# Kernel tuning notes

Hardware: AMD Instinct MI355X
Metric: run time of the kernel (lower is better)

## Reference

```python
import jax, jax.numpy as jnp
import numpy as np

EXP_SCALE = 10.0   # self.exp_param_scale
BETA_UP = 5.0      # self.kernel_beta_upbound
N_HEAD = 12


def setup_inputs() -> dict:
    key = jax.random.key(0)
    ks = jax.random.split(key, 7)
    B, T, C, nh = 2, 2048, 768, N_HEAD
    s = 1.0 / np.sqrt(C)
    x = jax.random.normal(ks[0], (B, T, C), jnp.float32)
    W_la = jax.random.normal(ks[1], (C, C), jnp.float32) * s      # LeakyAverage linear
    la_coef = jax.random.uniform(ks[2], (nh,), jnp.float32)        # per-head leaky decay in (0,1)
    W_v = jax.random.normal(ks[3], (C, C), jnp.float32) * s        # v_featurizer linear
    v_coef = jax.random.uniform(ks[4], (nh,), jnp.float32)         # v_featurizer per-head coef
    kernel_beta = jnp.ones((nh,), jnp.float32) / EXP_SCALE
    value_beta = jnp.ones((nh,), jnp.float32) * (-0.5 / EXP_SCALE)
    W_proj = jax.random.normal(ks[5], (C, C), jnp.float32) * s     # c_proj
    return dict(x=x, W_la=W_la, la_coef=la_coef, W_v=W_v, v_coef=v_coef,
                kernel_beta=kernel_beta, value_beta=value_beta, W_proj=W_proj)


def _leaky_average(x, W_la, la_coef):
    # y_t = c * y_{t-1} + (1-c) * (x W^T)_t, per-head decay c. Returns (B, nh, T, hs).
    B, T, C = x.shape
    nh = la_coef.shape[0]
    hs = C // nh
    u = (x @ W_la.T).reshape(B, T, nh, hs)
    c = la_coef[None, :, None]  # (1, nh, 1) broadcast over (B, nh, hs)

    def step(carry, ut):
        y = c * carry + (1.0 - c) * ut
        return y, y

    _, ys = jax.lax.scan(step, jnp.zeros((B, nh, hs), x.dtype), jnp.swapaxes(u, 0, 1))
    return jnp.transpose(ys, (1, 2, 0, 3))  # (T,B,nh,hs) -> (B,nh,T,hs)


def reference(x, W_la, la_coef, W_v, v_coef, kernel_beta, value_beta, W_proj):
    B, T, C = x.shape
    nh = la_coef.shape[0]
    hs = C // nh
    v_shift = 1

    # K path: leaky-average features, L2-normalize, exp-kernel beta scale
    k0 = _leaky_average(x, W_la, la_coef)                               # (B,nh,T,hs)
    raw_k = k0 / (jnp.linalg.norm(k0, axis=-1, keepdims=True) + 1e-6)
    beta = jnp.exp(jnp.minimum(kernel_beta * EXP_SCALE, BETA_UP))
    k = raw_k * beta[None, :, None, None]

    # V path: lowrlinearconv featurizer (linear, shift-by-1 mix, normalize) + value scale
    xl = (x @ W_v.T).reshape(B, T, nh, hs).transpose(0, 2, 1, 3)        # (B,nh,T,hs)
    shifted = jnp.concatenate([xl[:, :, 1:], jnp.zeros_like(xl[:, :, :1])], axis=2)
    vc = v_coef[None, :, None, None]
    vf = shifted * (1.0 - vc) + xl * vc
    vf = vf / (jnp.linalg.norm(vf, axis=-1, keepdims=True) + 1e-6)
    vbeta = jnp.exp(jnp.minimum(value_beta * EXP_SCALE, BETA_UP))
    v = vf * vbeta[None, :, None, None]

    # shifted-causal attention: query at position t (t>=1) attends keys 0..t-1, scale=1.0
    q = k[:, :, v_shift:]                                               # (B,nh,T-1,hs)
    scores = jnp.einsum('bhqd,bhkd->bhqk', q, k)                        # (B,nh,T-1,T)
    mask = jnp.tril(jnp.ones((T - v_shift, T), bool))                   # j <= iq  <=>  key < query pos
    scores = jnp.where(mask, scores, -jnp.inf)
    attn = jax.nn.softmax(scores, axis=-1)
    o = jnp.einsum('bhqk,bhkd->bhqd', attn, v)
    y = jnp.concatenate([jnp.zeros((B, nh, v_shift, hs), x.dtype), o], axis=2)

    y = y.transpose(0, 2, 1, 3).reshape(B, T, C)
    return y @ W_proj.T  # c_proj (dropouts are identity in eval)
```

## Files before the change

kernel.cpp:

```cpp
#include <hip/hip_runtime.h>
#include <hip/hip_bf16.h>
#include <math.h>

#define B_   2
#define T_   2048
#define C_   768
#define NH   12
#define HS   64
#define NSEG 64
#define SEGLEN 32
#define CX   1536

typedef __attribute__((ext_vector_type(8))) short short8;
typedef __attribute__((ext_vector_type(4))) short short4v;
typedef __attribute__((ext_vector_type(4))) float f32x4;

static __device__ inline unsigned short f2b(float f) {
  __hip_bfloat16 h = __float2bfloat16(f);
  unsigned short u;
  __builtin_memcpy(&u, &h, 2);
  return u;
}
static __device__ inline float b2f(unsigned short u) {
  unsigned int x = ((unsigned int)u) << 16;
  float f;
  __builtin_memcpy(&f, &x, 4);
  return f;
}

#define GLOAD_LDS16(gp, lp)                                                        \
  __builtin_amdgcn_global_load_lds((const __attribute__((address_space(1))) void*)(gp), \
                                   (__attribute__((address_space(3))) void*)(lp), 16, 0, 0)

__global__ __launch_bounds__(256) void cast_all(const float* __restrict__ x,
                                                const float* __restrict__ wla,
                                                const float* __restrict__ wv,
                                                const float* __restrict__ wp,
                                                __hip_bfloat16* __restrict__ xb,
                                                __hip_bfloat16* __restrict__ wcat,
                                                __hip_bfloat16* __restrict__ wpb) {
  const int NX4 = (B_ * T_ * C_) / 4;
  const int NW4 = (C_ * C_) / 4;
  const int TOT = NX4 + 3 * NW4;
  int i = blockIdx.x * 256 + threadIdx.x;
  int st = gridDim.x * 256;
  for (; i < TOT; i += st) {
    const float* s;
    unsigned short* d;
    if (i < NX4) { s = x + (size_t)i * 4; d = (unsigned short*)xb + (size_t)i * 4; }
    else if (i < NX4 + NW4) { int j = i - NX4; s = wla + (size_t)j * 4; d = (unsigned short*)wcat + (size_t)j * 4; }
    else if (i < NX4 + 2 * NW4) { int j = i - NX4 - NW4; s = wv + (size_t)j * 4; d = (unsigned short*)wcat + (size_t)(C_ * C_) + (size_t)j * 4; }
    else { int j = i - NX4 - 2 * NW4; s = wp + (size_t)j * 4; d = (unsigned short*)wpb + (size_t)j * 4; }
    float4 v = *(const float4*)s;
    short4v o;
    o.x = (short)f2b(v.x); o.y = (short)f2b(v.y); o.z = (short)f2b(v.z); o.w = (short)f2b(v.w);
    *(short4v*)d = o;
  }
}

template <int BM, bool OB16>
__global__ __launch_bounds__(256) void gemm_bf16(const __hip_bfloat16* __restrict__ A,
                                                 const __hip_bfloat16* __restrict__ Bw,
                                                 void* __restrict__ Cv,
                                                 int M, int N, int K) {
  __shared__ __hip_bfloat16 As[BM * 64];
  __shared__ __hip_bfloat16 Bs[128 * 64];
  const int tid = threadIdx.x;
  const int w = tid >> 6, lane = tid & 63;
  const int bm = blockIdx.x * BM, bn = blockIdx.y * 128;
  const int q16 = lane & 15, lg = lane >> 4;

  constexpr int NACC = (BM == 128) ? 4 : 2;
  f32x4 acc[4][NACC];
#pragma unroll
  for (int i = 0; i < 4; ++i)
#pragma unroll
    for (int j = 0; j < NACC; ++j) acc[i][j] = (f32x4){0.f, 0.f, 0.f, 0.f};

  const int srow = (lane >> 3);
  const int soff0 = (lane & 7) * 16;
  const int sw = (lane & 7) << 4;
  constexpr int ACH = BM / 8;
  constexpr int CPW = (ACH + 16) / 4;

  for (int k0 = 0; k0 < K; k0 += 64) {
    __syncthreads();
#pragma unroll
    for (int c = 0; c < CPW; ++c) {
      int gc = w * CPW + c;
      int isB = gc >= ACH;
      int ci = isB ? gc - ACH : gc;
      int row = ci * 8 + srow;
      int soff = soff0 ^ ((row & 7) << 4);
      const __hip_bfloat16* gp =
          (isB ? Bw + (size_t)(bn + row) * K : A + (size_t)(bm + row) * K) + k0 + (soff >> 1);
      __hip_bfloat16* lp = (isB ? Bs : As) + ci * 512;
      GLOAD_LDS16(gp, lp);
    }
    __syncthreads();
#pragma unroll
    for (int ks = 0; ks < 2; ++ks) {
      short8 af[4], bf[NACC];
      const int colb = ks * 64 + lg * 16;
#pragma unroll
      for (int i = 0; i < 4; ++i) {
        int ra = (BM == 128) ? ((w >> 1) * 64 + i * 16 + q16) : (i * 16 + q16);
        af[i] = *(const short8*)((const char*)As + ra * 128 + (colb ^ sw));
      }
#pragma unroll
      for (int j = 0; j < NACC; ++j) {
        int rb = (BM == 128) ? ((w & 1) * 64 + j * 16 + q16) : (w * 32 + j * 16 + q16);
        bf[j] = *(const short8*)((const char*)Bs + rb * 128 + (colb ^ sw));
      }
#pragma unroll
      for (int i = 0; i < 4; ++i)
#pragma unroll
        for (int j = 0; j < NACC; ++j)
          acc[i][j] = __builtin_amdgcn_mfma_f32_16x16x32_bf16(af[i], bf[j], acc[i][j], 0, 0, 0);
    }
  }
#pragma unroll
  for (int i = 0; i < 4; ++i) {
#pragma unroll
    for (int r = 0; r < 4; ++r) {
      int m = (BM == 128) ? (bm + (w >> 1) * 64 + i * 16 + lg * 4 + r)
                          : (bm + i * 16 + lg * 4 + r);
      int nb = (BM == 128) ? (bn + (w & 1) * 64 + q16) : (bn + w * 32 + q16);
      if (OB16) {
        unsigned short* cp = (unsigned short*)Cv + (size_t)m * N + nb;
#pragma unroll
        for (int j = 0; j < NACC; ++j) cp[j * 16] = f2b(acc[i][j][r]);
      } else {
        float* cp = (float*)Cv + (size_t)m * N + nb;
#pragma unroll
        for (int j = 0; j < NACC; ++j) cp[j * 16] = acc[i][j][r];
      }
    }
  }
}

__global__ __launch_bounds__(256) void scan_seg(const unsigned short* __restrict__ uxv,
                                                const float* __restrict__ la_coef,
                                                float* __restrict__ segend) {
  int cid = blockIdx.x * 4 + (threadIdx.x >> 6);
  int d   = threadIdx.x & 63;
  int seg = cid & (NSEG - 1);
  int bh  = cid >> 6;
  int h   = bh % NH;
  int b   = bh / NH;
  float c  = la_coef[h];
  float oc = 1.f - c;
  int t0 = seg * SEGLEN;
  const unsigned short* up = uxv + ((size_t)b * T_ + t0) * CX + h * HS + d;
  float uv[SEGLEN];
#pragma unroll
  for (int i = 0; i < SEGLEN; ++i) uv[i] = b2f(up[(size_t)i * CX]);
  float y = 0.f;
#pragma unroll
  for (int i = 0; i < SEGLEN; ++i) y = fmaf(c, y, oc * uv[i]);
  segend[(size_t)cid * HS + d] = y;
}

__global__ __launch_bounds__(256) void scanc_vbuild(const float* __restrict__ la_coef,
                                                    const float* __restrict__ kernel_beta,
                                                    const float* __restrict__ segend,
                                                    const unsigned short* __restrict__ uxv,
                                                    const float* __restrict__ v_coef,
                                                    const float* __restrict__ value_beta,
                                                    __hip_bfloat16* __restrict__ kb16,
                                                    __hip_bfloat16* __restrict__ vt) {
  __shared__ __hip_bfloat16 sm[64][73];
  const int NBC = B_ * NH * NSEG / 4;
  if ((int)blockIdx.x < NBC) {
    int cid = blockIdx.x * 4 + (threadIdx.x >> 6);
    int d   = threadIdx.x & 63;
    int seg = cid & (NSEG - 1);
    int bh  = cid >> 6;
    int h   = bh % NH;
    int b   = bh / NH;
    float c  = la_coef[h];
    float oc = 1.f - c;
    float bk = __expf(fminf(kernel_beta[h] * 10.f, 5.f));
    float cl = c;
#pragma unroll
    for (int i = 0; i < 5; ++i) cl *= cl;
    const float* se = segend + (size_t)bh * NSEG * HS + d;
    float y = 0.f;
    for (int s = 0; s < seg; ++s) y = fmaf(y, cl, se[(size_t)s * HS]);
    int t0 = seg * SEGLEN;
    const unsigned short* up = uxv + ((size_t)b * T_ + t0) * CX + h * HS + d;
    __hip_bfloat16* op = kb16 + ((size_t)bh * T_ + t0) * HS + d;
    float uv[SEGLEN];
#pragma unroll
    for (int i = 0; i < SEGLEN; ++i) uv[i] = b2f(up[(size_t)i * CX]);
    for (int i = 0; i < SEGLEN; ++i) {
      y = fmaf(c, y, oc * uv[i]);
      float ss = y * y;
#pragma unroll
      for (int off = 1; off < 64; off <<= 1) ss += __shfl_xor(ss, off, 64);
      float scale = bk / (sqrtf(ss) + 1e-6f);
      op[(size_t)i * HS] = __float2bfloat16(y * scale);
    }
  } else {
    int idx = blockIdx.x - NBC;
    int t0 = (idx & 31) * 64;
    int bh = idx >> 5;
    int h = bh % NH, b = bh / NH;
    int w = threadIdx.x >> 6, lane = threadIdx.x & 63;
    float vc = v_coef[h];
    float vb = __expf(fminf(value_beta[h] * 10.f, 5.f));
    for (int i = 0; i < 16; ++i) {
      int tl = w * 16 + i;
      int t = t0 + tl;
      const unsigned short* xp = uxv + ((size_t)b * T_ + t) * CX + 768 + h * HS + lane;
      float x0 = b2f(*xp);
      float x1 = (t + 1 < T_) ? b2f(xp[CX]) : 0.f;
      float vf = (1.f - vc) * x1 + vc * x0;
      float ss = vf * vf;
#pragma unroll
      for (int off = 1; off < 64; off <<= 1) ss += __shfl_xor(ss, off, 64);
      sm[tl][lane] = __float2bfloat16(vf * vb / (sqrtf(ss) + 1e-6f));
    }
    __syncthreads();
    int d = threadIdx.x >> 3;
    int c = threadIdx.x & 7;
    for (int i = 0; i < 2; ++i) {
      int dd = d + i * 32;
      short8 v;
#pragma unroll
      for (int k = 0; k < 8; ++k)
        v[k] = (short)((const unsigned short*)&sm[c * 8 + k][dd])[0];
      *(short8*)((unsigned short*)vt + ((size_t)bh * HS + dd) * T_ + t0 + c * 8) = v;
    }
  }
}

__global__ __launch_bounds__(256, 2) void attn8(const __hip_bfloat16* __restrict__ Kg,
                                                const __hip_bfloat16* __restrict__ Vtg,
                                                const float* __restrict__ kernel_beta,
                                                __hip_bfloat16* __restrict__ Y) {
  __shared__ __align__(16) char lds[38912];
  const int bh = blockIdx.x;
  const int b = bh / NH, h = bh % NH;
  const int w = threadIdx.x >> 6, lane = threadIdx.x & 63;
  const int q16 = lane & 15, lg = lane >> 4;
  const int it = 31 - blockIdx.y;
  const int qb0 = 1 + it * 64;
  const int NT32 = 2 * it + 2;
  float bk = __expf(fminf(kernel_beta[h] * 10.f, 5.f));
  const float L2E = 1.4426950408889634f;
  const float m0l = bk * bk * L2E;
  const unsigned short* Kh = (const unsigned short*)Kg + (size_t)bh * T_ * HS;
  const unsigned short* Vh = (const unsigned short*)Vtg + (size_t)bh * HS * T_;
  unsigned short* Yh = (unsigned short*)Y + (size_t)b * T_ * C_ + h * HS;

  if (it == 0 && w == 0) Yh[lane] = 0;

  short8 qf[4][2];
#pragma unroll
  for (int qs = 0; qs < 4; ++qs) {
    int tqc = qb0 + qs * 16 + q16;
    if (tqc > T_ - 1) tqc = T_ - 1;
#pragma unroll
    for (int ks = 0; ks < 2; ++ks)
      qf[qs][ks] = *(const short8*)(Kh + (size_t)tqc * HS + ks * 32 + lg * 8);
  }

  f32x4 zero = {0.f, 0.f, 0.f, 0.f};
  f32x4 accO[4][4];
#pragma unroll
  for (int qs = 0; qs < 4; ++qs)
#pragma unroll
    for (int mt = 0; mt < 4; ++mt) accO[qs][mt] = zero;
  float lsum[4] = {0.f, 0.f, 0.f, 0.f};
  char* pwbase = lds + (size_t)w * 4 * 1152;

#define LOADT(KF, VF, j0)                                                             \
  {                                                                                   \
    _Pragma("unroll")                                                                 \
    for (int nt = 0; nt < 2; ++nt)                                                    \
      _Pragma("unroll")                                                               \
      for (int ks = 0; ks < 2; ++ks)                                                  \
        KF[nt][ks] = *(const short8*)(Kh + (size_t)((j0) + nt * 16 + q16) * HS +      \
                                      ks * 32 + lg * 8);                              \
    _Pragma("unroll")                                                                 \
    for (int mt = 0; mt < 4; ++mt)                                                    \
      VF[mt] = *(const short8*)(Vh + (size_t)(mt * 16 + q16) * T_ + (j0) + lg * 8);   \
  }

#define COMPUTE(KF, VF, ktv)                                                          \
  {                                                                                   \
    const int j0c = (ktv)*32;                                                         \
    _Pragma("unroll")                                                                 \
    for (int qs = 0; qs < 4; ++qs) {                                                  \
      const int tqq = qb0 + qs * 16 + q16;                                            \
      char* pb = pwbase + qs * 1152 + q16 * 72;                                       \
      f32x4 s0 = __builtin_amdgcn_mfma_f32_16x16x32_bf16(KF[0][0], qf[qs][0], zero, 0, 0, 0); \
      s0 = __builtin_amdgcn_mfma_f32_16x16x32_bf16(KF[0][1], qf[qs][1], s0, 0, 0, 0); \
      f32x4 s1 = __builtin_amdgcn_mfma_f32_16x16x32_bf16(KF[1][0], qf[qs][0], zero, 0, 0, 0); \
      s1 = __builtin_amdgcn_mfma_f32_16x16x32_bf16(KF[1][1], qf[qs][1], s1, 0, 0, 0); \
      float p0[4], p1[4];                                                             \
      _Pragma("unroll")                                                               \
      for (int r = 0; r < 4; ++r) {                                                   \
        int j0r = j0c + lg * 4 + r;                                                   \
        p0[r] = (j0r < tqq) ? exp2f(fmaf(s0[r], L2E, -m0l)) : 0.f;                    \
        int j1r = j0c + 16 + lg * 4 + r;                                              \
        p1[r] = (j1r < tqq) ? exp2f(fmaf(s1[r], L2E, -m0l)) : 0.f;                    \
        lsum[qs] += p0[r] + p1[r];                                                    \
      }                                                                               \
      unsigned int w00, w01, w10, w11;                                                \
      asm("v_cvt_pk_bf16_f32 %0, %1, %2" : "=v"(w00) : "v"(p0[0]), "v"(p0[1]));       \
      asm("v_cvt_pk_bf16_f32 %0, %1, %2" : "=v"(w01) : "v"(p0[2]), "v"(p0[3]));       \
      asm("v_cvt_pk_bf16_f32 %0, %1, %2" : "=v"(w10) : "v"(p1[0]), "v"(p1[1]));       \
      asm("v_cvt_pk_bf16_f32 %0, %1, %2" : "=v"(w11) : "v"(p1[2]), "v"(p1[3]));       \
      uint2 pkA; pkA.x = w00; pkA.y = w01;                                            \
      uint2 pkB; pkB.x = w10; pkB.y = w11;                                            \
      *(uint2*)(pb + lg * 8) = pkA;                                                   \
      *(uint2*)(pb + 32 + lg * 8) = pkB;                                              \
      short8 pf = *(const short8*)(pb + lg * 16);                                     \
      _Pragma("unroll")                                                               \
      for (int mt = 0; mt < 4; ++mt)                                                  \
        accO[qs][mt] = __builtin_amdgcn_mfma_f32_16x16x32_bf16(VF[mt], pf, accO[qs][mt], 0, 0, 0); \
    }                                                                                 \
  }

  short8 kfA[2][2], vfA[4], kfB[2][2], vfB[4];
  int kt = w;
  if (kt < NT32) LOADT(kfA, vfA, kt * 32);
  while (kt < NT32) {
    if (kt + 4 < NT32) LOADT(kfB, vfB, (kt + 4) * 32);
    COMPUTE(kfA, vfA, kt);
    kt += 4;
    if (kt >= NT32) break;
    if (kt + 4 < NT32) LOADT(kfA, vfA, (kt + 4) * 32);
    COMPUTE(kfB, vfB, kt);
    kt += 4;
  }

  __syncthreads();
  float* LR = (float*)(lds + 34816);
  if (w >= 2) {
    float* PB = (float*)(lds + (size_t)(w - 2) * 17408);
#pragma unroll
    for (int qs = 0; qs < 4; ++qs)
#pragma unroll
      for (int mt = 0; mt < 4; ++mt)
        *(f32x4*)(PB + (qs * 16 + q16) * 68 + mt * 16 + lg * 4) = accO[qs][mt];
  }
#pragma unroll
  for (int qs = 0; qs < 4; ++qs)
    LR[((size_t)w * 64 + qs * 16 + q16) * 4 + lg] = lsum[qs];
  __syncthreads();
  if (w < 2) {
    float* PB = (float*)(lds + (size_t)w * 17408);
#pragma unroll
    for (int qs = 0; qs < 4; ++qs)
#pragma unroll
      for (int mt = 0; mt < 4; ++mt) {
        f32x4 o = *(f32x4*)(PB + (qs * 16 + q16) * 68 + mt * 16 + lg * 4);
        accO[qs][mt][0] += o[0]; accO[qs][mt][1] += o[1];
        accO[qs][mt][2] += o[2]; accO[qs][mt][3] += o[3];
      }
    if (w == 1) {
#pragma unroll
      for (int qs = 0; qs < 4; ++qs)
#pragma unroll
        for (int mt = 0; mt < 4; ++mt)
          *(f32x4*)(PB + (qs * 16 + q16) * 68 + mt * 16 + lg * 4) = accO[qs][mt];
    }
  }
  __syncthreads();
  if (w == 0) {
    float* PB1 = (float*)(lds + 17408);
#pragma unroll
    for (int qs = 0; qs < 4; ++qs) {
#pragma unroll
      for (int mt = 0; mt < 4; ++mt) {
        f32x4 o = *(f32x4*)(PB1 + (qs * 16 + q16) * 68 + mt * 16 + lg * 4);
        accO[qs][mt][0] += o[0]; accO[qs][mt][1] += o[1];
        accO[qs][mt][2] += o[2]; accO[qs][mt][3] += o[3];
      }
      float tot = 0.f;
#pragma unroll
      for (int p = 0; p < 4; ++p) {
        f32x4 lv = *(f32x4*)(LR + ((size_t)p * 64 + qs * 16 + q16) * 4);
        tot += lv[0] + lv[1] + lv[2] + lv[3];
      }
      float inv = 1.f / tot;
      int tq = qb0 + qs * 16 + q16;
      if (tq < T_) {
        unsigned short* yp = Yh + (size_t)tq * C_;
#pragma unroll
        for (int mt = 0; mt < 4; ++mt) {
          float o0 = accO[qs][mt][0] * inv, o1 = accO[qs][mt][1] * inv;
          float o2 = accO[qs][mt][2] * inv, o3 = accO[qs][mt][3] * inv;
          unsigned int u0, u1;
          asm("v_cvt_pk_bf16_f32 %0, %1, %2" : "=v"(u0) : "v"(o0), "v"(o1));
          asm("v_cvt_pk_bf16_f32 %0, %1, %2" : "=v"(u1) : "v"(o2), "v"(o3));
          uint2 pk; pk.x = u0; pk.y = u1;
          *(uint2*)(yp + mt * 16 + lg * 4) = pk;
        }
      }
    }
  }
#undef LOADT
#undef COMPUTE
}

extern "C" void kernel_launch(void* const* d_in, const int* in_sizes, int n_in,
                              void* d_out, int out_size, void* d_ws, size_t ws_size,
                              hipStream_t stream) {
  const float* x          = (const float*)d_in[0];
  const float* W_la       = (const float*)d_in[1];
  const float* la_coef    = (const float*)d_in[2];
  const float* W_v        = (const float*)d_in[3];
  const float* v_coef     = (const float*)d_in[4];
  const float* kernel_bet = (const float*)d_in[5];
  const float* value_bet  = (const float*)d_in[6];
  const float* W_proj     = (const float*)d_in[7];
  float* out = (float*)d_out;

  char* ws = (char*)d_ws;
  const size_t NTOK = (size_t)B_ * T_ * C_;
  const size_t NSEGTOT = (size_t)B_ * NH * NSEG * HS;
  unsigned short* uxv = (unsigned short*)ws;
  float* segend  = (float*)(ws + (size_t)B_ * T_ * CX * 2);
  __hip_bfloat16* kb16 = (__hip_bfloat16*)(segend + NSEGTOT);
  __hip_bfloat16* vt16 = kb16 + NTOK;
  __hip_bfloat16* xb   = vt16 + NTOK;
  __hip_bfloat16* Wcat = xb + NTOK;
  __hip_bfloat16* Wpb  = Wcat + (size_t)CX * C_;
  __hip_bfloat16* yb   = xb;

  const int M = B_ * T_;

  cast_all<<<2048, 256, 0, stream>>>(x, W_la, W_v, W_proj, xb, Wcat, Wpb);

  gemm_bf16<64, true><<<dim3(M / 64, CX / 128), 256, 0, stream>>>(xb, Wcat, uxv, M, CX, C_);

  scan_seg<<<dim3(B_ * NH * NSEG / 4), 256, 0, stream>>>(uxv, la_coef, segend);
  scanc_vbuild<<<dim3(B_ * NH * NSEG / 4 + 32 * B_ * NH), 256, 0, stream>>>(
      la_coef, kernel_bet, segend, uxv, v_coef, value_bet, kb16, vt16);

  attn8<<<dim3(B_ * NH, 32), 256, 0, stream>>>(kb16, vt16, kernel_bet, yb);

  gemm_bf16<64, false><<<dim3(M / 64, C_ / 128), 256, 0, stream>>>(yb, Wpb, out, M, C_, C_);
}
```

Measured before the change: 110.3 us.

## Precompute scan carries, skip masking on full tiles, shrink attention LDS reduction

Adds a small kernel that computes each segment's carry-in state once, so each scan chunk no longer re-walks all prior segment ends serially. In the attention kernel, key tiles lying entirely below the causal diagonal skip the per-element mask comparisons. The cross-wave output reduction becomes a sequential accumulate through one shared buffer, which cuts LDS use so three blocks can fit per CU. The cost is an extra kernel launch and more barriers in the reduction.

```diff
diff --git a/kernel.cpp b/kernel.cpp
--- a/kernel.cpp
+++ b/kernel.cpp
@@ -161,9 +161,29 @@
   segend[(size_t)cid * HS + d] = y;
 }
 
+__global__ __launch_bounds__(256) void scan_b(const float* __restrict__ la_coef,
+                                              const float* __restrict__ segend,
+                                              float* __restrict__ carryin) {
+  int s = blockIdx.x * 256 + threadIdx.x;
+  if (s >= B_ * NH * HS) return;
+  int d  = s & 63;
+  int bh = s >> 6;
+  int h  = bh % NH;
+  float c = la_coef[h];
+  float cl = c;
+#pragma unroll
+  for (int i = 0; i < 5; ++i) cl *= cl;
+  float h0 = 0.f;
+  for (int seg = 0; seg < NSEG; ++seg) {
+    int cid = bh * NSEG + seg;
+    carryin[(size_t)cid * HS + d] = h0;
+    h0 = fmaf(cl, h0, segend[(size_t)cid * HS + d]);
+  }
+}
+
 __global__ __launch_bounds__(256) void scanc_vbuild(const float* __restrict__ la_coef,
                                                     const float* __restrict__ kernel_beta,
-                                                    const float* __restrict__ segend,
+                                                    const float* __restrict__ carryin,
                                                     const unsigned short* __restrict__ uxv,
                                                     const float* __restrict__ v_coef,
                                                     const float* __restrict__ value_beta,
@@ -181,18 +201,13 @@
     float c  = la_coef[h];
     float oc = 1.f - c;
     float bk = __expf(fminf(kernel_beta[h] * 10.f, 5.f));
-    float cl = c;
-#pragma unroll
-    for (int i = 0; i < 5; ++i) cl *= cl;
-    const float* se = segend + (size_t)bh * NSEG * HS + d;
-    float y = 0.f;
-    for (int s = 0; s < seg; ++s) y = fmaf(y, cl, se[(size_t)s * HS]);
     int t0 = seg * SEGLEN;
     const unsigned short* up = uxv + ((size_t)b * T_ + t0) * CX + h * HS + d;
     __hip_bfloat16* op = kb16 + ((size_t)bh * T_ + t0) * HS + d;
     float uv[SEGLEN];
 #pragma unroll
     for (int i = 0; i < SEGLEN; ++i) uv[i] = b2f(up[(size_t)i * CX]);
+    float y = carryin[(size_t)cid * HS + d];
     for (int i = 0; i < SEGLEN; ++i) {
       y = fmaf(c, y, oc * uv[i]);
       float ss = y * y;
@@ -235,11 +250,11 @@
   }
 }
 
-__global__ __launch_bounds__(256, 2) void attn8(const __hip_bfloat16* __restrict__ Kg,
+__global__ __launch_bounds__(256, 3) void attn9(const __hip_bfloat16* __restrict__ Kg,
                                                 const __hip_bfloat16* __restrict__ Vtg,
                                                 const float* __restrict__ kernel_beta,
                                                 __hip_bfloat16* __restrict__ Y) {
-  __shared__ __align__(16) char lds[38912];
+  __shared__ __align__(16) char lds[18432];
   const int bh = blockIdx.x;
   const int b = bh / NH, h = bh % NH;
   const int w = threadIdx.x >> 6, lane = threadIdx.x & 63;
@@ -294,19 +309,29 @@
     _Pragma("unroll")                                                                 \
     for (int qs = 0; qs < 4; ++qs) {                                                  \
       const int tqq = qb0 + qs * 16 + q16;                                            \
+      const bool unmasked = (j0c + 32 <= qb0 + qs * 16);            \
       char* pb = pwbase + qs * 1152 + q16 * 72;                                       \
       f32x4 s0 = __builtin_amdgcn_mfma_f32_16x16x32_bf16(KF[0][0], qf[qs][0], zero, 0, 0, 0); \
       s0 = __builtin_amdgcn_mfma_f32_16x16x32_bf16(KF[0][1], qf[qs][1], s0, 0, 0, 0); \
       f32x4 s1 = __builtin_amdgcn_mfma_f32_16x16x32_bf16(KF[1][0], qf[qs][0], zero, 0, 0, 0); \
       s1 = __builtin_amdgcn_mfma_f32_16x16x32_bf16(KF[1][1], qf[qs][1], s1, 0, 0, 0); \
       float p0[4], p1[4];                                                             \
-      _Pragma("unroll")                                                               \
-      for (int r = 0; r < 4; ++r) {                                                   \
-        int j0r = j0c + lg * 4 + r;                                                   \
-        p0[r] = (j0r < tqq) ? exp2f(fmaf(s0[r], L2E, -m0l)) : 0.f;                    \
-        int j1r = j0c + 16 + lg * 4 + r;                                              \
-        p1[r] = (j1r < tqq) ? exp2f(fmaf(s1[r], L2E, -m0l)) : 0.f;                    \
-        lsum[qs] += p0[r] + p1[r];                                                    \
+      if (unmasked) {                                                                 \
+        _Pragma("unroll")                                                             \
+        for (int r = 0; r < 4; ++r) {                                                 \
+          p0[r] = exp2f(fmaf(s0[r], L2E, -m0l));                                      \
+          p1[r] = exp2f(fmaf(s1[r], L2E, -m0l));                                      \
+          lsum[qs] += p0[r] + p1[r];                                                  \
+        }                                                                             \
+      } else {                                                                        \
+        _Pragma("unroll")                                                             \
+        for (int r = 0; r < 4; ++r) {                                                 \
+          int j0r = j0c + lg * 4 + r;                                                 \
+          p0[r] = (j0r < tqq) ? exp2f(fmaf(s0[r], L2E, -m0l)) : 0.f;                  \
+          int j1r = j0c + 16 + lg * 4 + r;                                            \
+          p1[r] = (j1r < tqq) ? exp2f(fmaf(s1[r], L2E, -m0l)) : 0.f;                  \
+          lsum[qs] += p0[r] + p1[r];                                                  \
+        }                                                                             \
       }                                                                               \
       unsigned int w00, w01, w10, w11;                                                \
       asm("v_cvt_pk_bf16_f32 %0, %1, %2" : "=v"(w00) : "v"(p0[0]), "v"(p0[1]));       \
@@ -338,55 +363,61 @@
   }
 
   __syncthreads();
-  float* LR = (float*)(lds + 34816);
-  if (w >= 2) {
-    float* PB = (float*)(lds + (size_t)(w - 2) * 17408);
-#pragma unroll
-    for (int qs = 0; qs < 4; ++qs)
+  float* PB = (float*)lds;
+  if (w == 3) {
+#pragma unroll
+    for (int qs = 0; qs < 4; ++qs) {
+      float* rb = PB + (qs * 16 + q16) * 72;
 #pragma unroll
       for (int mt = 0; mt < 4; ++mt)
-        *(f32x4*)(PB + (qs * 16 + q16) * 68 + mt * 16 + lg * 4) = accO[qs][mt];
-  }
-#pragma unroll
-  for (int qs = 0; qs < 4; ++qs)
-    LR[((size_t)w * 64 + qs * 16 + q16) * 4 + lg] = lsum[qs];
+        *(f32x4*)(rb + mt * 16 + lg * 4) = accO[qs][mt];
+      rb[64 + lg] = lsum[qs];
+    }
+  }
   __syncthreads();
-  if (w < 2) {
-    float* PB = (float*)(lds + (size_t)w * 17408);
-#pragma unroll
-    for (int qs = 0; qs < 4; ++qs)
+  if (w == 2) {
+#pragma unroll
+    for (int qs = 0; qs < 4; ++qs) {
+      float* rb = PB + (qs * 16 + q16) * 72;
 #pragma unroll
       for (int mt = 0; mt < 4; ++mt) {
-        f32x4 o = *(f32x4*)(PB + (qs * 16 + q16) * 68 + mt * 16 + lg * 4);
+        f32x4 o = *(f32x4*)(rb + mt * 16 + lg * 4);
+        o[0] += accO[qs][mt][0]; o[1] += accO[qs][mt][1];
+        o[2] += accO[qs][mt][2]; o[3] += accO[qs][mt][3];
+        *(f32x4*)(rb + mt * 16 + lg * 4) = o;
+      }
+      rb[64 + lg] += lsum[qs];
+    }
+  }
+  __syncthreads();
+  if (w == 1) {
+#pragma unroll
+    for (int qs = 0; qs < 4; ++qs) {
+      float* rb = PB + (qs * 16 + q16) * 72;
+#pragma unroll
+      for (int mt = 0; mt < 4; ++mt) {
+        f32x4 o = *(f32x4*)(rb + mt * 16 + lg * 4);
+        o[0] += accO[qs][mt][0]; o[1] += accO[qs][mt][1];
+        o[2] += accO[qs][mt][2]; o[3] += accO[qs][mt][3];
+        *(f32x4*)(rb + mt * 16 + lg * 4) = o;
+      }
+      rb[64 + lg] += lsum[qs];
+    }
+  }
+  __syncthreads();
+  if (w == 0) {
+#pragma unroll
+    for (int qs = 0; qs < 4; ++qs) {
+      float* rb = PB + (qs * 16 + q16) * 72;
+#pragma unroll
+      for (int mt = 0; mt < 4; ++mt) {
+        f32x4 o = *(f32x4*)(rb + mt * 16 + lg * 4);
         accO[qs][mt][0] += o[0]; accO[qs][mt][1] += o[1];
         accO[qs][mt][2] += o[2]; accO[qs][mt][3] += o[3];
       }
-    if (w == 1) {
-#pragma unroll
-      for (int qs = 0; qs < 4; ++qs)
-#pragma unroll
-        for (int mt = 0; mt < 4; ++mt)
-          *(f32x4*)(PB + (qs * 16 + q16) * 68 + mt * 16 + lg * 4) = accO[qs][mt];
-    }
-  }
-  __syncthreads();
-  if (w == 0) {
-    float* PB1 = (float*)(lds + 17408);
-#pragma unroll
-    for (int qs = 0; qs < 4; ++qs) {
-#pragma unroll
-      for (int mt = 0; mt < 4; ++mt) {
-        f32x4 o = *(f32x4*)(PB1 + (qs * 16 + q16) * 68 + mt * 16 + lg * 4);
-        accO[qs][mt][0] += o[0]; accO[qs][mt][1] += o[1];
-        accO[qs][mt][2] += o[2]; accO[qs][mt][3] += o[3];
-      }
-      float tot = 0.f;
-#pragma unroll
-      for (int p = 0; p < 4; ++p) {
-        f32x4 lv = *(f32x4*)(LR + ((size_t)p * 64 + qs * 16 + q16) * 4);
-        tot += lv[0] + lv[1] + lv[2] + lv[3];
-      }
-      float inv = 1.f / tot;
+      rb[64 + lg] += lsum[qs];
+      f32x4 lv = *(f32x4*)(rb + 64);
+      float inv = 1.f / (lv[0] + lv[1] + lv[2] + lv[3]);
       int tq = qb0 + qs * 16 + q16;
       if (tq < T_) {
         unsigned short* yp = Yh + (size_t)tq * C_;
@@ -425,7 +456,8 @@
   const size_t NSEGTOT = (size_t)B_ * NH * NSEG * HS;
   unsigned short* uxv = (unsigned short*)ws;
   float* segend  = (float*)(ws + (size_t)B_ * T_ * CX * 2);
-  __hip_bfloat16* kb16 = (__hip_bfloat16*)(segend + NSEGTOT);
+  float* carryin = segend + NSEGTOT;
+  __hip_bfloat16* kb16 = (__hip_bfloat16*)(carryin + NSEGTOT);
   __hip_bfloat16* vt16 = kb16 + NTOK;
   __hip_bfloat16* xb   = vt16 + NTOK;
   __hip_bfloat16* Wcat = xb + NTOK;
@@ -439,10 +471,11 @@
   gemm_bf16<64, true><<<dim3(M / 64, CX / 128), 256, 0, stream>>>(xb, Wcat, uxv, M, CX, C_);
 
   scan_seg<<<dim3(B_ * NH * NSEG / 4), 256, 0, stream>>>(uxv, la_coef, segend);
+  scan_b<<<dim3((B_ * NH * HS + 255) / 256), 256, 0, stream>>>(la_coef, segend, carryin);
   scanc_vbuild<<<dim3(B_ * NH * NSEG / 4 + 32 * B_ * NH), 256, 0, stream>>>(
-      la_coef, kernel_bet, segend, uxv, v_coef, value_bet, kb16, vt16);
-
-  attn8<<<dim3(B_ * NH, 32), 256, 0, stream>>>(kb16, vt16, kernel_bet, yb);
+      la_coef, kernel_bet, carryin, uxv, v_coef, value_bet, kb16, vt16);
+
+  attn9<<<dim3(B_ * NH, 32), 256, 0, stream>>>(kb16, vt16, kernel_bet, yb);
 
   gemm_bf16<64, false><<<dim3(M / 64, C_ / 128), 256, 0, stream>>>(yb, Wpb, out, M, C_, C_);
 }
```

Result: slower. 227.3 us (+106.1%).

## Switch attention to 32x32 MFMA with permlane P-reshuffle; precompute segment carries

Applied to the files above, without the earlier changes.

The attention kernel is rewritten to use 32x32x16 bf16 MFMAs over 32-query tiles. The softmax probabilities are rearranged into the B-operand layout with permlane32_swap in registers instead of a round trip through LDS, and s_setprio is placed around the MFMA groups. Separately, a new small scan kernel computes per-segment carry-in values once, so each scanc block no longer loops serially over all earlier segment ends. This adds one more kernel launch, and the larger accumulators raise register pressure.

```diff
diff --git a/kernel.cpp b/kernel.cpp
--- a/kernel.cpp
+++ b/kernel.cpp
@@ -14,6 +14,9 @@
 typedef __attribute__((ext_vector_type(8))) short short8;
 typedef __attribute__((ext_vector_type(4))) short short4v;
 typedef __attribute__((ext_vector_type(4))) float f32x4;
+typedef __attribute__((ext_vector_type(16))) float f32x16;
+typedef __attribute__((ext_vector_type(2))) unsigned int uint2v;
+typedef __attribute__((ext_vector_type(4))) unsigned int uint4v;
 
 static __device__ inline unsigned short f2b(float f) {
   __hip_bfloat16 h = __float2bfloat16(f);
@@ -26,6 +29,11 @@
   float f;
   __builtin_memcpy(&f, &x, 4);
   return f;
+}
+static __device__ inline unsigned cvtpk(float a, float b) {
+  unsigned r;
+  asm("v_cvt_pk_bf16_f32 %0, %1, %2" : "=v"(r) : "v"(a), "v"(b));
+  return r;
 }
 
 #define GLOAD_LDS16(gp, lp)                                                        \
@@ -161,9 +169,29 @@
   segend[(size_t)cid * HS + d] = y;
 }
 
+__global__ __launch_bounds__(256) void scan_b(const float* __restrict__ la_coef,
+                                              const float* __restrict__ segend,
+                                              float* __restrict__ carryin) {
+  int s = blockIdx.x * 256 + threadIdx.x;
+  if (s >= B_ * NH * HS) return;
+  int d  = s & 63;
+  int bh = s >> 6;
+  int h  = bh % NH;
+  float c = la_coef[h];
+  float cl = c;
+#pragma unroll
+  for (int i = 0; i < 5; ++i) cl *= cl;
+  float h0 = 0.f;
+  for (int seg = 0; seg < NSEG; ++seg) {
+    int cid = bh * NSEG + seg;
+    carryin[(size_t)cid * HS + d] = h0;
+    h0 = fmaf(cl, h0, segend[(size_t)cid * HS + d]);
+  }
+}
+
 __global__ __launch_bounds__(256) void scanc_vbuild(const float* __restrict__ la_coef,
                                                     const float* __restrict__ kernel_beta,
-                                                    const float* __restrict__ segend,
+                                                    const float* __restrict__ carryin,
                                                     const unsigned short* __restrict__ uxv,
                                                     const float* __restrict__ v_coef,
                                                     const float* __restrict__ value_beta,
@@ -181,18 +209,13 @@
     float c  = la_coef[h];
     float oc = 1.f - c;
     float bk = __expf(fminf(kernel_beta[h] * 10.f, 5.f));
-    float cl = c;
-#pragma unroll
-    for (int i = 0; i < 5; ++i) cl *= cl;
-    const float* se = segend + (size_t)bh * NSEG * HS + d;
-    float y = 0.f;
-    for (int s = 0; s < seg; ++s) y = fmaf(y, cl, se[(size_t)s * HS]);
     int t0 = seg * SEGLEN;
     const unsigned short* up = uxv + ((size_t)b * T_ + t0) * CX + h * HS + d;
     __hip_bfloat16* op = kb16 + ((size_t)bh * T_ + t0) * HS + d;
     float uv[SEGLEN];
 #pragma unroll
     for (int i = 0; i < SEGLEN; ++i) uv[i] = b2f(up[(size_t)i * CX]);
+    float y = carryin[(size_t)cid * HS + d];
     for (int i = 0; i < SEGLEN; ++i) {
       y = fmaf(c, y, oc * uv[i]);
       float ss = y * y;
@@ -235,15 +258,15 @@
   }
 }
 
-__global__ __launch_bounds__(256, 2) void attn8(const __hip_bfloat16* __restrict__ Kg,
-                                                const __hip_bfloat16* __restrict__ Vtg,
-                                                const float* __restrict__ kernel_beta,
-                                                __hip_bfloat16* __restrict__ Y) {
-  __shared__ __align__(16) char lds[38912];
+__global__ __launch_bounds__(256, 2) void attn10(const __hip_bfloat16* __restrict__ Kg,
+                                                 const __hip_bfloat16* __restrict__ Vtg,
+                                                 const float* __restrict__ kernel_beta,
+                                                 __hip_bfloat16* __restrict__ Y) {
+  __shared__ __align__(16) char lds[33792];
   const int bh = blockIdx.x;
   const int b = bh / NH, h = bh % NH;
   const int w = threadIdx.x >> 6, lane = threadIdx.x & 63;
-  const int q16 = lane & 15, lg = lane >> 4;
+  const int l31 = lane & 31, lg2 = lane >> 5;
   const int it = 31 - blockIdx.y;
   const int qb0 = 1 + it * 64;
   const int NT32 = 2 * it + 2;
@@ -256,75 +279,83 @@
 
   if (it == 0 && w == 0) Yh[lane] = 0;
 
-  short8 qf[4][2];
-#pragma unroll
-  for (int qs = 0; qs < 4; ++qs) {
-    int tqc = qb0 + qs * 16 + q16;
+  short8 qf[2][4];
+#pragma unroll
+  for (int qs = 0; qs < 2; ++qs) {
+    int tqc = qb0 + qs * 32 + l31;
     if (tqc > T_ - 1) tqc = T_ - 1;
 #pragma unroll
-    for (int ks = 0; ks < 2; ++ks)
-      qf[qs][ks] = *(const short8*)(Kh + (size_t)tqc * HS + ks * 32 + lg * 8);
-  }
-
-  f32x4 zero = {0.f, 0.f, 0.f, 0.f};
-  f32x4 accO[4][4];
-#pragma unroll
-  for (int qs = 0; qs < 4; ++qs)
-#pragma unroll
-    for (int mt = 0; mt < 4; ++mt) accO[qs][mt] = zero;
-  float lsum[4] = {0.f, 0.f, 0.f, 0.f};
-  char* pwbase = lds + (size_t)w * 4 * 1152;
+    for (int s = 0; s < 4; ++s)
+      qf[qs][s] = *(const short8*)(Kh + (size_t)tqc * HS + s * 16 + lg2 * 8);
+  }
+
+  f32x16 zero16 = {0.f};
+  f32x16 accO[2][2];
+#pragma unroll
+  for (int qs = 0; qs < 2; ++qs)
+#pragma unroll
+    for (int ds = 0; ds < 2; ++ds) accO[qs][ds] = zero16;
+  float lsum[2] = {0.f, 0.f};
 
 #define LOADT(KF, VF, j0)                                                             \
   {                                                                                   \
     _Pragma("unroll")                                                                 \
-    for (int nt = 0; nt < 2; ++nt)                                                    \
+    for (int s = 0; s < 4; ++s)                                                       \
+      KF[s] = *(const short8*)(Kh + (size_t)((j0) + l31) * HS + s * 16 + lg2 * 8);    \
+    _Pragma("unroll")                                                                 \
+    for (int ds = 0; ds < 2; ++ds)                                                    \
       _Pragma("unroll")                                                               \
-      for (int ks = 0; ks < 2; ++ks)                                                  \
-        KF[nt][ks] = *(const short8*)(Kh + (size_t)((j0) + nt * 16 + q16) * HS +      \
-                                      ks * 32 + lg * 8);                              \
-    _Pragma("unroll")                                                                 \
-    for (int mt = 0; mt < 4; ++mt)                                                    \
-      VF[mt] = *(const short8*)(Vh + (size_t)(mt * 16 + q16) * T_ + (j0) + lg * 8);   \
+      for (int s2 = 0; s2 < 2; ++s2)                                                  \
+        VF[ds][s2] = *(const short8*)(Vh + (size_t)(ds * 32 + l31) * T_ + (j0) +      \
+                                      s2 * 16 + lg2 * 8);                             \
   }
 
 #define COMPUTE(KF, VF, ktv)                                                          \
   {                                                                                   \
     const int j0c = (ktv)*32;                                                         \
+    const int jb = j0c + 4 * lg2;                                                     \
     _Pragma("unroll")                                                                 \
-    for (int qs = 0; qs < 4; ++qs) {                                                  \
-      const int tqq = qb0 + qs * 16 + q16;                                            \
-      char* pb = pwbase + qs * 1152 + q16 * 72;                                       \
-      f32x4 s0 = __builtin_amdgcn_mfma_f32_16x16x32_bf16(KF[0][0], qf[qs][0], zero, 0, 0, 0); \
-      s0 = __builtin_amdgcn_mfma_f32_16x16x32_bf16(KF[0][1], qf[qs][1], s0, 0, 0, 0); \
-      f32x4 s1 = __builtin_amdgcn_mfma_f32_16x16x32_bf16(KF[1][0], qf[qs][0], zero, 0, 0, 0); \
-      s1 = __builtin_amdgcn_mfma_f32_16x16x32_bf16(KF[1][1], qf[qs][1], s1, 0, 0, 0); \
-      float p0[4], p1[4];                                                             \
+    for (int qs = 0; qs < 2; ++qs) {                                                  \
+      const int tqq = qb0 + qs * 32 + l31;                                            \
+      f32x16 S = zero16;                                                              \
+      __builtin_amdgcn_s_setprio(1);                                                  \
       _Pragma("unroll")                                                               \
-      for (int r = 0; r < 4; ++r) {                                                   \
-        int j0r = j0c + lg * 4 + r;                                                   \
-        p0[r] = (j0r < tqq) ? exp2f(fmaf(s0[r], L2E, -m0l)) : 0.f;                    \
-        int j1r = j0c + 16 + lg * 4 + r;                                              \
-        p1[r] = (j1r < tqq) ? exp2f(fmaf(s1[r], L2E, -m0l)) : 0.f;                    \
-        lsum[qs] += p0[r] + p1[r];                                                    \
+      for (int s = 0; s < 4; ++s)                                                     \
+        S = __builtin_amdgcn_mfma_f32_32x32x16_bf16(KF[s], qf[qs][s], S, 0, 0, 0);    \
+      __builtin_amdgcn_s_setprio(0);                                                  \
+      float p[16];                                                                    \
+      _Pragma("unroll")                                                               \
+      for (int r = 0; r < 16; ++r) {                                                  \
+        int jg = jb + (r & 3) + 8 * (r >> 2);                                         \
+        p[r] = (jg < tqq) ? exp2f(fmaf(S[r], L2E, -m0l)) : 0.f;                       \
+        lsum[qs] += p[r];                                                             \
       }                                                                               \
-      unsigned int w00, w01, w10, w11;                                                \
-      asm("v_cvt_pk_bf16_f32 %0, %1, %2" : "=v"(w00) : "v"(p0[0]), "v"(p0[1]));       \
-      asm("v_cvt_pk_bf16_f32 %0, %1, %2" : "=v"(w01) : "v"(p0[2]), "v"(p0[3]));       \
-      asm("v_cvt_pk_bf16_f32 %0, %1, %2" : "=v"(w10) : "v"(p1[0]), "v"(p1[1]));       \
-      asm("v_cvt_pk_bf16_f32 %0, %1, %2" : "=v"(w11) : "v"(p1[2]), "v"(p1[3]));       \
-      uint2 pkA; pkA.x = w00; pkA.y = w01;                                            \
-      uint2 pkB; pkB.x = w10; pkB.y = w11;                                            \
-      *(uint2*)(pb + lg * 8) = pkA;                                                   \
-      *(uint2*)(pb + 32 + lg * 8) = pkB;                                              \
-      short8 pf = *(const short8*)(pb + lg * 16);                                     \
+      uint2v g00 = __builtin_amdgcn_permlane32_swap(cvtpk(p[0], p[1]),                \
+                                                    cvtpk(p[4], p[5]), false, false); \
+      uint2v g01 = __builtin_amdgcn_permlane32_swap(cvtpk(p[2], p[3]),                \
+                                                    cvtpk(p[6], p[7]), false, false); \
+      uint2v g10 = __builtin_amdgcn_permlane32_swap(cvtpk(p[8], p[9]),                \
+                                                    cvtpk(p[12], p[13]), false, false);\
+      uint2v g11 = __builtin_amdgcn_permlane32_swap(cvtpk(p[10], p[11]),              \
+                                                    cvtpk(p[14], p[15]), false, false);\
+      uint4v pb0v, pb1v;                                                              \
+      pb0v.x = g00.x; pb0v.y = g01.x; pb0v.z = g00.y; pb0v.w = g01.y;                 \
+      pb1v.x = g10.x; pb1v.y = g11.x; pb1v.z = g10.y; pb1v.w = g11.y;                 \
+      short8 PB0 = __builtin_bit_cast(short8, pb0v);                                  \
+      short8 PB1 = __builtin_bit_cast(short8, pb1v);                                  \
+      __builtin_amdgcn_s_setprio(1);                                                  \
       _Pragma("unroll")                                                               \
-      for (int mt = 0; mt < 4; ++mt)                                                  \
-        accO[qs][mt] = __builtin_amdgcn_mfma_f32_16x16x32_bf16(VF[mt], pf, accO[qs][mt], 0, 0, 0); \
+      for (int ds = 0; ds < 2; ++ds) {                                                \
+        accO[qs][ds] = __builtin_amdgcn_mfma_f32_32x32x16_bf16(VF[ds][0], PB0,        \
+                                                               accO[qs][ds], 0, 0, 0);\
+        accO[qs][ds] = __builtin_amdgcn_mfma_f32_32x32x16_bf16(VF[ds][1], PB1,        \
+                                                               accO[qs][ds], 0, 0, 0);\
+      }                                                                               \
+      __builtin_amdgcn_s_setprio(0);                                                  \
     }                                                                                 \
   }
 
-  short8 kfA[2][2], vfA[4], kfB[2][2], vfB[4];
+  short8 kfA[4], vfA[2][2], kfB[4], vfB[2][2];
   int kt = w;
   if (kt < NT32) LOADT(kfA, vfA, kt * 32);
   while (kt < NT32) {
@@ -337,69 +368,65 @@
     kt += 4;
   }
 
+#pragma unroll
+  for (int qs = 0; qs < 2; ++qs) lsum[qs] += __shfl_xor(lsum[qs], 32, 64);
+
+  float* LR = (float*)(lds + 32768);
   __syncthreads();
-  float* LR = (float*)(lds + 34816);
   if (w >= 2) {
-    float* PB = (float*)(lds + (size_t)(w - 2) * 17408);
-#pragma unroll
-    for (int qs = 0; qs < 4; ++qs)
-#pragma unroll
-      for (int mt = 0; mt < 4; ++mt)
-        *(f32x4*)(PB + (qs * 16 + q16) * 68 + mt * 16 + lg * 4) = accO[qs][mt];
-  }
-#pragma unroll
-  for (int qs = 0; qs < 4; ++qs)
-    LR[((size_t)w * 64 + qs * 16 + q16) * 4 + lg] = lsum[qs];
+    float* PB = (float*)(lds + (size_t)(w - 2) * 16384);
+#pragma unroll
+    for (int qs = 0; qs < 2; ++qs)
+#pragma unroll
+      for (int ds = 0; ds < 2; ++ds)
+        *(f32x16*)(PB + ((qs * 2 + ds) * 64 + lane) * 16) = accO[qs][ds];
+  }
+#pragma unroll
+  for (int qs = 0; qs < 2; ++qs) LR[(w * 2 + qs) * 32 + l31] = lsum[qs];
   __syncthreads();
   if (w < 2) {
-    float* PB = (float*)(lds + (size_t)w * 17408);
-#pragma unroll
-    for (int qs = 0; qs < 4; ++qs)
-#pragma unroll
-      for (int mt = 0; mt < 4; ++mt) {
-        f32x4 o = *(f32x4*)(PB + (qs * 16 + q16) * 68 + mt * 16 + lg * 4);
-        accO[qs][mt][0] += o[0]; accO[qs][mt][1] += o[1];
-        accO[qs][mt][2] += o[2]; accO[qs][mt][3] += o[3];
+    float* PB = (float*)(lds + (size_t)w * 16384);
+#pragma unroll
+    for (int qs = 0; qs < 2; ++qs)
+#pragma unroll
+      for (int ds = 0; ds < 2; ++ds) {
+        f32x16 o = *(f32x16*)(PB + ((qs * 2 + ds) * 64 + lane) * 16);
+#pragma unroll
+        for (int r = 0; r < 16; ++r) accO[qs][ds][r] += o[r];
       }
     if (w == 1) {
 #pragma unroll
-      for (int qs = 0; qs < 4; ++qs)
-#pragma unroll
-        for (int mt = 0; mt < 4; ++mt)
-          *(f32x4*)(PB + (qs * 16 + q16) * 68 + mt * 16 + lg * 4) = accO[qs][mt];
+      for (int qs = 0; qs < 2; ++qs)
+#pragma unroll
+        for (int ds = 0; ds < 2; ++ds)
+          *(f32x16*)(PB + ((qs * 2 + ds) * 64 + lane) * 16) = accO[qs][ds];
     }
   }
   __syncthreads();
   if (w == 0) {
-    float* PB1 = (float*)(lds + 17408);
-#pragma unroll
-    for (int qs = 0; qs < 4; ++qs) {
-#pragma unroll
-      for (int mt = 0; mt < 4; ++mt) {
-        f32x4 o = *(f32x4*)(PB1 + (qs * 16 + q16) * 68 + mt * 16 + lg * 4);
-        accO[qs][mt][0] += o[0]; accO[qs][mt][1] += o[1];
-        accO[qs][mt][2] += o[2]; accO[qs][mt][3] += o[3];
-      }
-      float tot = 0.f;
-#pragma unroll
-      for (int p = 0; p < 4; ++p) {
-        f32x4 lv = *(f32x4*)(LR + ((size_t)p * 64 + qs * 16 + q16) * 4);
-        tot += lv[0] + lv[1] + lv[2] + lv[3];
-      }
+    float* PB1 = (float*)(lds + 16384);
+#pragma unroll
+    for (int qs = 0; qs < 2; ++qs) {
+#pragma unroll
+      for (int ds = 0; ds < 2; ++ds) {
+        f32x16 o = *(f32x16*)(PB1 + ((qs * 2 + ds) * 64 + lane) * 16);
+#pragma unroll
+        for (int r = 0; r < 16; ++r) accO[qs][ds][r] += o[r];
+      }
+      float tot = LR[(0 * 2 + qs) * 32 + l31] + LR[(1 * 2 + qs) * 32 + l31] +
+                  LR[(2 * 2 + qs) * 32 + l31] + LR[(3 * 2 + qs) * 32 + l31];
       float inv = 1.f / tot;
-      int tq = qb0 + qs * 16 + q16;
+      int tq = qb0 + qs * 32 + l31;
       if (tq < T_) {
         unsigned short* yp = Yh + (size_t)tq * C_;
 #pragma unroll
-        for (int mt = 0; mt < 4; ++mt) {
-          float o0 = accO[qs][mt][0] * inv, o1 = accO[qs][mt][1] * inv;
-          float o2 = accO[qs][mt][2] * inv, o3 = accO[qs][mt][3] * inv;
-          unsigned int u0, u1;
-          asm("v_cvt_pk_bf16_f32 %0, %1, %2" : "=v"(u0) : "v"(o0), "v"(o1));
-          asm("v_cvt_pk_bf16_f32 %0, %1, %2" : "=v"(u1) : "v"(o2), "v"(o3));
-          uint2 pk; pk.x = u0; pk.y = u1;
-          *(uint2*)(yp + mt * 16 + lg * 4) = pk;
-        }
+        for (int ds = 0; ds < 2; ++ds)
+#pragma unroll
+          for (int r = 0; r < 16; r += 2) {
+            int d = ds * 32 + (r & 3) + 8 * (r >> 2) + 4 * lg2;
+            unsigned u = cvtpk(accO[qs][ds][r] * inv, accO[qs][ds][r + 1] * inv);
+            *(unsigned*)(yp + d) = u;
+          }
       }
     }
   }
@@ -425,7 +452,8 @@
   const size_t NSEGTOT = (size_t)B_ * NH * NSEG * HS;
   unsigned short* uxv = (unsigned short*)ws;
   float* segend  = (float*)(ws + (size_t)B_ * T_ * CX * 2);
-  __hip_bfloat16* kb16 = (__hip_bfloat16*)(segend + NSEGTOT);
+  float* carryin = segend + NSEGTOT;
+  __hip_bfloat16* kb16 = (__hip_bfloat16*)(carryin + NSEGTOT);
   __hip_bfloat16* vt16 = kb16 + NTOK;
   __hip_bfloat16* xb   = vt16 + NTOK;
   __hip_bfloat16* Wcat = xb + NTOK;
@@ -439,10 +467,11 @@
   gemm_bf16<64, true><<<dim3(M / 64, CX / 128), 256, 0, stream>>>(xb, Wcat, uxv, M, CX, C_);
 
   scan_seg<<<dim3(B_ * NH * NSEG / 4), 256, 0, stream>>>(uxv, la_coef, segend);
+  scan_b<<<dim3((B_ * NH * HS + 255) / 256), 256, 0, stream>>>(la_coef, segend, carryin);
   scanc_vbuild<<<dim3(B_ * NH * NSEG / 4 + 32 * B_ * NH), 256, 0, stream>>>(
-      la_coef, kernel_bet, segend, uxv, v_coef, value_bet, kb16, vt16);
-
-  attn8<<<dim3(B_ * NH, 32), 256, 0, stream>>>(kb16, vt16, kernel_bet, yb);
+      la_coef, kernel_bet, carryin, uxv, v_coef, value_bet, kb16, vt16);
+
+  attn10<<<dim3(B_ * NH, 32), 256, 0, stream>>>(kb16, vt16, kernel_bet, yb);
 
   gemm_bf16<64, false><<<dim3(M / 64, C_ / 128), 256, 0, stream>>>(yb, Wpb, out, M, C_, C_);
 }
```

Result: faster. 101.1 us (-8.3%).
